# Kernel optimization log

Hardware: AMD Instinct MI355X
Metric: run time of the kernel (lower is better)

## Reference

```python
import jax, jax.numpy as jnp
import numpy as np
import math

H, C = 16, 4


def _clustering(x, alv, mu, log_var, log_prior, mi_estimation):
    # x: [B,h,L,D], alv: [B,h,L], mu/log_var: [h or 1, C, D], log_prior: [h or 1, C]
    B, Hh, L, D = x.shape
    z = x  # eval mode: no reparameterization noise
    zd = z[:, :, :, None, :]                       # [B,h,L,1,D]
    mu_b = mu[:, None, :, :]                       # [h,1,C,D]
    lv = log_var[:, None, :, :]
    var = jnp.exp(lv)
    lp = jax.nn.log_softmax(log_prior, axis=-1)    # [h,C]
    mse = (zd - mu_b) ** 2 / var                   # [B,h,L,C,D]
    log_pdf = -0.5 * mse.sum(-1) - 0.5 * lv.sum(-1) - D * math.pi  # [B,h,L,C]
    log_pdf = log_pdf + lp[:, None, :]
    shift = jax.lax.stop_gradient(log_pdf.max(axis=-1, keepdims=True))
    log_probs = jax.nn.log_softmax(log_pdf - shift + 5.0, axis=-1)
    cp = jnp.exp(log_probs)                        # cluster probs [B,h,L,C]
    lp_b = jnp.broadcast_to(lp[None, :, None, :], log_probs.shape)
    # F.kl_div(log_probs, prior) = prior * (log prior - log_probs)
    kl = (jnp.exp(lp_b) * (lp_b - log_probs)).sum(-1).mean(axis=(1, 2))
    alv5 = alv[:, :, :, None, None]
    avar = jnp.exp(alv5)
    kl = kl + 0.5 * (cp * (mse + avar / var + lv).sum(-1)).sum(-1).mean(axis=(1, 2))
    kl = kl - 0.5 * ((1.0 + alv5).sum(-1) * D).mean(axis=(1, 2, 3))
    eye = jnp.eye(L, dtype=x.dtype)
    div = jnp.einsum('bhqc,bhkc->bhqk', cp, cp)
    div = ((div - eye) ** 2) * (eye * 1.25 + (1.0 - eye) * 0.75)
    div_loss = div.mean(axis=(1, 2, 3))
    if mi_estimation:
        pdf = jnp.exp(log_pdf - jax.lax.stop_gradient(log_pdf.max())).sum(-1, keepdims=True)
        w = cp * pdf
        mi_probs = w / jnp.maximum(w.sum(axis=2, keepdims=True), 1e-6)  # L1 normalize over L
        mi_p = jnp.minimum(jnp.einsum('bilc,bjlc->blij', mi_probs, cp), 1.0)
        mask_h = 1.0 - jnp.eye(Hh, dtype=x.dtype)
        mi_loss = -(jnp.log(1.0 - mi_p + 1e-6) * mask_h).mean(axis=(1, 2, 3)) * 10.0
        aff = jnp.einsum('bhqc,bhkc->bhqk', cp, cp)
        diag = jnp.diagonal(jax.nn.log_softmax(aff, axis=-1), axis1=2, axis2=3)
        mi_loss = mi_loss - diag.mean(axis=(1, 2))
    else:
        mi_loss = jnp.zeros_like(kl)
    return z, cp, kl, div_loss, mi_loss


def _forward(query, key, value, Wq, bq, Wk, bk, Wv, bv, Wo, bo, Wsem, bsem,
             Whead, bhead, tok_mu, tok_log_var, tok_log_prior,
             head_mu, head_log_var, head_log_prior):
    B, L, D = query.shape
    Dk = D // H
    q = query @ Wq + bq
    k = key @ Wk + bk
    v = value @ Wv + bv
    alv = (q @ Wsem + bsem).transpose(0, 2, 1)                 # [B,H,L]
    qh = q.reshape(B, L, H, Dk).transpose(0, 2, 1, 3)          # [B,H,L,Dk]
    z, cp_q, kl_q, div_q, _ = _clustering(qh, alv, tok_mu, tok_log_var, tok_log_prior, False)
    kh = k.reshape(B, L, H, Dk).transpose(0, 2, 1, 3)
    vh = v.reshape(B, L, H, Dk).transpose(0, 2, 1, 3)
    cluster_mask = jnp.einsum('bhqc,bhkc->bhqk', cp_q, cp_q)   # token-cluster affinity mask
    scores = jnp.einsum('bhqd,bhkd->bhqk', z, kh) / math.sqrt(Dk)
    attn = jax.nn.softmax(scores, axis=-1) * cluster_mask
    attn = attn / (attn.sum(axis=-1, keepdims=True) + 1e-6)
    ctx = jnp.einsum('bhqk,bhkd->bhqd', attn, vh)              # [B,H,L,Dk]
    ctx_f = ctx.transpose(0, 2, 1, 3).reshape(B, L, D)
    alv_h = (ctx_f @ Whead + bhead).transpose(0, 2, 1)         # [B,H,L]
    _, cp_h, kl_h, div_h, mi = _clustering(ctx, alv_h, head_mu, head_log_var, head_log_prior, True)
    out = ctx_f @ Wo + bo
    return out, attn.mean(axis=1), kl_q + kl_h, div_q + div_h, mi


def setup_inputs() -> dict:
    key = jax.random.key(0)
    ks = jax.random.split(key, 12)
    B, L, D = 8, 512, 1024
    Dk = D // H
    s = 1.0 / math.sqrt(D)
    f32 = jnp.float32
    inp = {
        'query': jax.random.normal(ks[0], (B, L, D), f32),
        'key': jax.random.normal(ks[1], (B, L, D), f32),
        'value': jax.random.normal(ks[2], (B, L, D), f32),
        'Wq': jax.random.normal(ks[3], (D, D), f32) * s, 'bq': jnp.zeros((D,), f32),
        'Wk': jax.random.normal(ks[4], (D, D), f32) * s, 'bk': jnp.zeros((D,), f32),
        'Wv': jax.random.normal(ks[5], (D, D), f32) * s, 'bv': jnp.zeros((D,), f32),
        'Wo': jax.random.normal(ks[6], (D, D), f32) * s, 'bo': jnp.zeros((D,), f32),
        'Wsem': jax.random.normal(ks[7], (D, H), f32) * s, 'bsem': jnp.zeros((H,), f32),
        'Whead': jax.random.normal(ks[8], (D, H), f32) * s, 'bhead': jnp.zeros((H,), f32),
        'tok_mu': jax.random.normal(ks[9], (H, C, Dk), f32) * 0.1,
        'tok_log_var': jnp.zeros((H, C, Dk), f32),
        'tok_log_prior': jnp.full((H, C), math.log(1.0 / C), f32),
        'head_mu': jax.random.normal(ks[10], (1, C, Dk), f32) * 0.1,
        'head_log_var': jnp.zeros((1, C, Dk), f32),
        'head_log_prior': jnp.full((1, C), math.log(1.0 / C), f32),
    }
    return inp


def reference(query, key, value, Wq, bq, Wk, bk, Wv, bv, Wo, bo, Wsem, bsem,
              Whead, bhead, tok_mu, tok_log_var, tok_log_prior,
              head_mu, head_log_var, head_log_prior):
    return _forward(query, key, value, Wq, bq, Wk, bk, Wv, bv, Wo, bo, Wsem, bsem,
                    Whead, bhead, tok_mu, tok_log_var, tok_log_prior,
                    head_mu, head_log_var, head_log_prior)
```

## Files before the change

kernel.cpp:

```cpp
#include <hip/hip_runtime.h>
#include <math.h>

#define BB 8
#define LL 512
#define DD 1024
#define HH 16
#define CC 4
#define DK 64
#define NEG_DPI 201.06192982974676f

typedef __attribute__((ext_vector_type(8))) short short8;
typedef __attribute__((ext_vector_type(4))) float floatx4;
typedef __attribute__((ext_vector_type(8))) unsigned short u16x8;
typedef __attribute__((ext_vector_type(4))) unsigned short u16x4;

__device__ inline float block_sum256(float v, float* s_red) {
    int t = threadIdx.x;
    s_red[t] = v; __syncthreads();
    for (int off = 128; off > 0; off >>= 1) {
        if (t < off) s_red[t] += s_red[t + off];
        __syncthreads();
    }
    float r = s_red[0]; __syncthreads();
    return r;
}
__device__ inline float block_max256(float v, float* s_red) {
    int t = threadIdx.x;
    s_red[t] = v; __syncthreads();
    for (int off = 128; off > 0; off >>= 1) {
        if (t < off) s_red[t] = fmaxf(s_red[t], s_red[t + off]);
        __syncthreads();
    }
    float r = s_red[0]; __syncthreads();
    return r;
}
__device__ inline unsigned int fenc(float f) {
    unsigned int b = __float_as_uint(f);
    return (b & 0x80000000u) ? ~b : (b | 0x80000000u);
}
__device__ inline float fdec(unsigned int u) {
    return (u & 0x80000000u) ? __uint_as_float(u ^ 0x80000000u) : __uint_as_float(~u);
}
__device__ inline unsigned short f2bf(float x) {
    unsigned int u = __float_as_uint(x);
    return (unsigned short)((u + 0x7FFFu + ((u >> 16) & 1u)) >> 16);
}
__device__ inline float bf2f(unsigned short h) {
    return __uint_as_float((unsigned int)h << 16);
}

__global__ __launch_bounds__(256)
void convert_hilo(const float* __restrict__ x, unsigned short* __restrict__ hh,
                  unsigned short* __restrict__ ll) {
    int i = blockIdx.x * 256 + threadIdx.x;
    float4 v = ((const float4*)x)[i];
    u16x4 h, l;
    float c[4] = {v.x, v.y, v.z, v.w};
#pragma unroll
    for (int j = 0; j < 4; j++) {
        unsigned short hb = f2bf(c[j]);
        h[j] = hb;
        l[j] = f2bf(c[j] - bf2f(hb));
    }
    ((u16x4*)hh)[i] = h;
    ((u16x4*)ll)[i] = l;
}

__global__ __launch_bounds__(256)
void wconv_kernel(const float* __restrict__ W, unsigned short* __restrict__ Th,
                  unsigned short* __restrict__ Tl) {
    __shared__ float tile[64][65];
    int t = threadIdx.x;
    int n0 = blockIdx.x * 64, k0 = blockIdx.y * 64;
    int r = t >> 4, c4 = (t & 15) * 4;
#pragma unroll
    for (int rr = 0; rr < 64; rr += 16) {
        float4 v = *(const float4*)&W[(size_t)(k0 + r + rr) * DD + n0 + c4];
        tile[r + rr][c4 + 0] = v.x; tile[r + rr][c4 + 1] = v.y;
        tile[r + rr][c4 + 2] = v.z; tile[r + rr][c4 + 3] = v.w;
    }
    __syncthreads();
    int rn = t >> 2, kg = (t & 3) * 16;
    u16x8 oh[2], ol[2];
#pragma unroll
    for (int j = 0; j < 16; j++) {
        float x = tile[kg + j][rn];
        unsigned short hb = f2bf(x);
        oh[j >> 3][j & 7] = hb;
        ol[j >> 3][j & 7] = f2bf(x - bf2f(hb));
    }
    size_t o = (size_t)(n0 + rn) * DD + k0 + kg;
    *(u16x8*)&Th[o] = oh[0]; *(u16x8*)&Th[o + 8] = oh[1];
    *(u16x8*)&Tl[o] = ol[0]; *(u16x8*)&Tl[o + 8] = ol[1];
}

__global__ __launch_bounds__(256)
void mfma_gemm_bias(const unsigned short* __restrict__ Ah, const unsigned short* __restrict__ Al,
                    const unsigned short* __restrict__ Bh, const unsigned short* __restrict__ Bl,
                    const float* __restrict__ bias, float* __restrict__ C,
                    unsigned short* __restrict__ Ch, unsigned short* __restrict__ Cl) {
    __shared__ unsigned short sAh[128 * 32];
    __shared__ unsigned short sAl[128 * 32];
    __shared__ unsigned short sBh[128 * 32];
    __shared__ unsigned short sBl[128 * 32];
    int t = threadIdx.x;
    int n0 = blockIdx.x * 128, m0 = blockIdx.y * 128;
    int lane = t & 63, w = t >> 6;
    int wm = w >> 1, wn = w & 1;
    int lm = lane & 15, quad = lane >> 4;
    int srow = t >> 1, sk = (t & 1) * 16;

    const unsigned short* gAh = Ah + (size_t)(m0 + srow) * DD + sk;
    const unsigned short* gAl = Al + (size_t)(m0 + srow) * DD + sk;
    const unsigned short* gBh = Bh + (size_t)(n0 + srow) * DD + sk;
    const unsigned short* gBl = Bl + (size_t)(n0 + srow) * DD + sk;
    unsigned short* wAh = &sAh[srow * 32 + sk];
    unsigned short* wAl = &sAl[srow * 32 + sk];
    unsigned short* wBh = &sBh[srow * 32 + sk];
    unsigned short* wBl = &sBl[srow * 32 + sk];

    floatx4 acc[4][4] = {};

    for (int kt = 0; kt < 32; kt++) {
        int kb = kt * 32;
        u16x8 a0 = *(const u16x8*)(gAh + kb);
        u16x8 a1 = *(const u16x8*)(gAh + kb + 8);
        u16x8 a2 = *(const u16x8*)(gAl + kb);
        u16x8 a3 = *(const u16x8*)(gAl + kb + 8);
        u16x8 b0 = *(const u16x8*)(gBh + kb);
        u16x8 b1 = *(const u16x8*)(gBh + kb + 8);
        u16x8 b2 = *(const u16x8*)(gBl + kb);
        u16x8 b3 = *(const u16x8*)(gBl + kb + 8);
        __syncthreads();
        *(u16x8*)(wAh) = a0; *(u16x8*)(wAh + 8) = a1;
        *(u16x8*)(wAl) = a2; *(u16x8*)(wAl + 8) = a3;
        *(u16x8*)(wBh) = b0; *(u16x8*)(wBh + 8) = b1;
        *(u16x8*)(wBl) = b2; *(u16x8*)(wBl + 8) = b3;
        __syncthreads();

        short8 bh[4], bl[4];
#pragma unroll
        for (int j = 0; j < 4; j++) {
            int nb = (wn * 64 + j * 16 + lm) * 32 + quad * 8;
            bh[j] = *(const short8*)&sBh[nb];
            bl[j] = *(const short8*)&sBl[nb];
        }
#pragma unroll
        for (int i = 0; i < 4; i++) {
            int ab = (wm * 64 + i * 16 + lm) * 32 + quad * 8;
            short8 ah = *(const short8*)&sAh[ab];
            short8 al = *(const short8*)&sAl[ab];
#pragma unroll
            for (int j = 0; j < 4; j++) {
                acc[i][j] = __builtin_amdgcn_mfma_f32_16x16x32_bf16(ah, bh[j], acc[i][j], 0, 0, 0);
                acc[i][j] = __builtin_amdgcn_mfma_f32_16x16x32_bf16(ah, bl[j], acc[i][j], 0, 0, 0);
                acc[i][j] = __builtin_amdgcn_mfma_f32_16x16x32_bf16(al, bh[j], acc[i][j], 0, 0, 0);
            }
        }
    }
#pragma unroll
    for (int i = 0; i < 4; i++) {
#pragma unroll
        for (int j = 0; j < 4; j++) {
            int n = n0 + wn * 64 + j * 16 + lm;
            float bv = bias[n];
#pragma unroll
            for (int r = 0; r < 4; r++) {
                int m = m0 + wm * 64 + i * 16 + quad * 4 + r;
                size_t idx = (size_t)m * DD + n;
                float val = acc[i][j][r] + bv;
                if (C) C[idx] = val;
                if (Ch) {
                    unsigned short hb = f2bf(val);
                    Ch[idx] = hb;
                    Cl[idx] = f2bf(val - bf2f(hb));
                }
            }
        }
    }
}

__global__ __launch_bounds__(256)
void vt_prep(const unsigned short* __restrict__ src, unsigned short* __restrict__ dst) {
    __shared__ unsigned short tile[128 * 68];
    int t = threadIdx.x;
    int l0 = blockIdx.x * 128, h = blockIdx.y, b = blockIdx.z;
#pragma unroll
    for (int i = 0; i < 8; i++) {
        int u = t + i * 256;
        int l = u >> 4, c4 = (u & 15) * 4;
        u16x4 v4 = *(const u16x4*)&src[((size_t)(b * LL + l0 + l)) * DD + h * DK + c4];
        tile[l * 68 + c4 + 0] = v4[0]; tile[l * 68 + c4 + 1] = v4[1];
        tile[l * 68 + c4 + 2] = v4[2]; tile[l * 68 + c4 + 3] = v4[3];
    }
    __syncthreads();
    size_t ob = ((size_t)(b * HH + h)) * DK * LL;
#pragma unroll
    for (int i = 0; i < 8; i++) {
        int u = t + i * 256;
        int d = u >> 5, lq = (u & 31) * 4;
        u16x4 o;
#pragma unroll
        for (int j = 0; j < 4; j++) o[j] = tile[(lq + j) * 68 + d];
        *(u16x4*)&dst[ob + (size_t)d * LL + l0 + lq] = o;
    }
}

__global__ __launch_bounds__(256)
void alv_gemm(const float* __restrict__ A, const float* __restrict__ Wp,
              const float* __restrict__ bias, float* __restrict__ alv) {
    __shared__ float As[16][65];
    __shared__ float Ws[64][17];
    int t = threadIdx.x;
    int m0 = blockIdx.x * 16;
    int r = t >> 4, hh = t & 15;
    float acc = 0.f;
    for (int kt = 0; kt < 16; kt++) {
        __syncthreads();
#pragma unroll
        for (int i = 0; i < 4; i++) {
            int e = t + i * 256;
            int rr = e >> 6, kk = e & 63;
            As[rr][kk] = A[(size_t)(m0 + rr) * DD + kt * 64 + kk];
        }
#pragma unroll
        for (int i = 0; i < 4; i++) {
            int e = t + i * 256;
            int kk = e >> 4, h2 = e & 15;
            Ws[kk][h2] = Wp[(size_t)(kt * 64 + kk) * HH + h2];
        }
        __syncthreads();
#pragma unroll
        for (int kk = 0; kk < 64; kk++) acc += As[r][kk] * Ws[kk][hh];
    }
    int m = m0 + r;
    int b = m >> 9, l = m & 511;
    alv[(size_t)(b * HH + hh) * LL + l] = acc + bias[hh];
}

__global__ __launch_bounds__(256)
void cluster_kernel(const float* __restrict__ zsrc, const float* __restrict__ alv,
                    const float* __restrict__ mu, const float* __restrict__ logvar,
                    const float* __restrict__ logprior,
                    float* __restrict__ cp_out, float* __restrict__ lpdf_out,
                    unsigned int* __restrict__ maxenc, float* __restrict__ kl_out,
                    int isHead) {
    __shared__ float s_mu[CC * DK], s_iv[CC * DK], s_lv[CC * DK];
    __shared__ float s_slv[CC], s_siv[CC], s_lp[CC];
    __shared__ float s_red[256];
    int t = threadIdx.x;
    int tile = blockIdx.x & 1;
    int bh = blockIdx.x >> 1;
    int h = bh & (HH - 1), b = bh >> 4;
    int hm = isHead ? 0 : h;

    {
        float m = mu[hm * CC * DK + t];
        float lv = logvar[hm * CC * DK + t];
        s_mu[t] = m; s_lv[t] = lv; s_iv[t] = expf(-lv);
    }
    __syncthreads();
    if (t < CC) {
        float slv = 0.f, siv = 0.f;
        for (int d = 0; d < DK; d++) { slv += s_lv[t * DK + d]; siv += s_iv[t * DK + d]; }
        s_slv[t] = slv; s_siv[t] = siv;
    }
    if (t == CC) {
        float x[CC];
        float m = -1e30f;
        for (int c = 0; c < CC; c++) { x[c] = logprior[hm * CC + c]; m = fmaxf(m, x[c]); }
        float se = 0.f;
        for (int c = 0; c < CC; c++) se += expf(x[c] - m);
        float lse = m + logf(se);
        for (int c = 0; c < CC; c++) s_lp[c] = x[c] - lse;
    }
    __syncthreads();

    int l = tile * 256 + t;
    const float* zp = zsrc + ((size_t)(b * LL + l)) * DD + h * DK;
    float acc[CC] = {0.f, 0.f, 0.f, 0.f};
    for (int d = 0; d < DK; d += 4) {
        float4 z4 = *(const float4*)(zp + d);
#pragma unroll
        for (int c = 0; c < CC; c++) {
            float d0 = z4.x - s_mu[c * DK + d];     acc[c] += d0 * d0 * s_iv[c * DK + d];
            float d1 = z4.y - s_mu[c * DK + d + 1]; acc[c] += d1 * d1 * s_iv[c * DK + d + 1];
            float d2 = z4.z - s_mu[c * DK + d + 2]; acc[c] += d2 * d2 * s_iv[c * DK + d + 2];
            float d3 = z4.w - s_mu[c * DK + d + 3]; acc[c] += d3 * d3 * s_iv[c * DK + d + 3];
        }
    }
    float lpdf[CC];
#pragma unroll
    for (int c = 0; c < CC; c++)
        lpdf[c] = -0.5f * acc[c] - 0.5f * s_slv[c] - NEG_DPI + s_lp[c];
    float m = fmaxf(fmaxf(lpdf[0], lpdf[1]), fmaxf(lpdf[2], lpdf[3]));
    float se = 0.f;
#pragma unroll
    for (int c = 0; c < CC; c++) se += expf(lpdf[c] - m);
    float lse = m + logf(se);
    float lprob[CC], cpv[CC];
    size_t idx = ((size_t)(bh * LL + l)) * CC;
#pragma unroll
    for (int c = 0; c < CC; c++) {
        lprob[c] = lpdf[c] - lse;
        cpv[c] = expf(lprob[c]);
        cp_out[idx + c] = cpv[c];
    }
    if (isHead) {
#pragma unroll
        for (int c = 0; c < CC; c++) lpdf_out[idx + c] = lpdf[c];
    }
    float alvv = alv[(size_t)bh * LL + l];
    float avar = expf(alvv);
    float t1 = 0.f, t2 = 0.f;
#pragma unroll
    for (int c = 0; c < CC; c++) {
        t1 += expf(s_lp[c]) * (s_lp[c] - lprob[c]);
        t2 += cpv[c] * (acc[c] + avar * s_siv[c] + s_slv[c]);
    }
    float klv = t1 + 0.5f * t2 - 0.5f * (float)DK * (1.0f + alvv);
    float tot = block_sum256(klv, s_red);
    if (t == 0) atomicAdd(kl_out + b, tot * (1.0f / (HH * LL)));
    if (isHead) {
        float mt = block_max256(m, s_red);
        if (t == 0) atomicMax(maxenc, fenc(mt));
    }
}

__global__ __launch_bounds__(256)
void pairstats_kernel(const float* __restrict__ cp, float* __restrict__ div_out,
                      float* __restrict__ mi_out, int isHead) {
    __shared__ float s_cp[LL * CC];
    __shared__ float s_red[256];
    int t = threadIdx.x;
    int bh = blockIdx.x >> 3;
    int seg = blockIdx.x & 7;
    int b = bh >> 4;
    const float* base = cp + (size_t)bh * LL * CC;
#pragma unroll
    for (int i = 0; i < 2; i++) {
        int e = t + i * 256;
        *(float4*)&s_cp[e * 4] = *(const float4*)&base[e * 4];
    }
    __syncthreads();

    int q = seg * 64 + (t >> 2);
    int ln = t & 3;
    float4 cq = *(float4*)&s_cp[q * 4];
    float divacc = 0.f, m = -1e30f, s = 0.f, selfdot = 0.f;
    for (int k = ln; k < LL; k += 4) {
        float4 ck = *(float4*)&s_cp[k * 4];
        float dot = cq.x * ck.x + cq.y * ck.y + cq.z * ck.z + cq.w * ck.w;
        float del = (k == q) ? 1.f : 0.f;
        float dd = dot - del;
        divacc += dd * dd * (0.75f + 0.5f * del);
        if (isHead) {
            if (dot > m) { s = s * expf(m - dot) + 1.f; m = dot; }
            else         { s += expf(dot - m); }
            if (k == q) selfdot = dot;
        }
    }
#pragma unroll
    for (int off = 1; off <= 2; off <<= 1) divacc += __shfl_xor(divacc, off, 64);
    float diag = 0.f;
    if (isHead) {
#pragma unroll
        for (int off = 1; off <= 2; off <<= 1) {
            float om = __shfl_xor(m, off, 64);
            float os = __shfl_xor(s, off, 64);
            float nm = fmaxf(m, om);
            s = s * expf(m - nm) + os * expf(om - nm);
            m = nm;
        }
#pragma unroll
        for (int off = 1; off <= 2; off <<= 1) selfdot += __shfl_xor(selfdot, off, 64);
        diag = selfdot - (m + logf(s));
    }
    float dtot = block_sum256(ln == 0 ? divacc : 0.f, s_red);
    if (t == 0) atomicAdd(div_out + b, dtot * (1.0f / ((float)HH * LL * LL)));
    if (isHead) {
        float gtot = block_sum256(ln == 0 ? diag : 0.f, s_red);
        if (t == 0) atomicAdd(mi_out + b, -gtot * (1.0f / (HH * LL)));
    }
}

__global__ __launch_bounds__(256)
void attn3_kernel(const unsigned short* __restrict__ qoh, const unsigned short* __restrict__ qol,
                  const unsigned short* __restrict__ koh, const unsigned short* __restrict__ kol,
                  const unsigned short* __restrict__ vth, const unsigned short* __restrict__ vtl,
                  const float* __restrict__ cpq,
                  float* __restrict__ ctxf, float* __restrict__ attn_h, int h0) {
    __shared__ __align__(16) char sbuf[33280];
    __shared__ float s_cp[LL * CC];
    __shared__ float s_inv[16];
    float* S = (float*)sbuf;
    unsigned short* Ph = (unsigned short*)sbuf;
    unsigned short* Pl = Ph + 16 * 520;

    int t = threadIdx.x;
    int qt = blockIdx.x, hl = blockIdx.y, b = blockIdx.z;
    int h = h0 + hl;
    int q0 = qt * 16;
    int lane = t & 63, w = t >> 6;
    int lm = lane & 15, quad = lane >> 4;
    int bh = b * HH + h;

    {
        const float* cpb = cpq + (size_t)bh * LL * CC;
#pragma unroll
        for (int i = 0; i < 2; i++) {
            int e = t + i * 256;
            *(float4*)&s_cp[e * 4] = *(const float4*)&cpb[e * 4];
        }
    }

    size_t qbase = ((size_t)(b * LL + q0 + lm)) * DD + h * DK + quad * 8;
    short8 qah0 = *(const short8*)(qoh + qbase);
    short8 qah1 = *(const short8*)(qoh + qbase + 32);
    short8 qal0 = *(const short8*)(qol + qbase);
    short8 qal1 = *(const short8*)(qol + qbase + 32);

    floatx4 sa[8] = {};
#pragma unroll
    for (int j = 0; j < 8; j++) {
        int n0 = w * 128 + j * 16;
        size_t kbase = ((size_t)(b * LL + n0 + lm)) * DD + h * DK + quad * 8;
        short8 kbh0 = *(const short8*)(koh + kbase);
        short8 kbh1 = *(const short8*)(koh + kbase + 32);
        short8 kbl0 = *(const short8*)(kol + kbase);
        short8 kbl1 = *(const short8*)(kol + kbase + 32);
        sa[j] = __builtin_amdgcn_mfma_f32_16x16x32_bf16(qah0, kbh0, sa[j], 0, 0, 0);
        sa[j] = __builtin_amdgcn_mfma_f32_16x16x32_bf16(qah1, kbh1, sa[j], 0, 0, 0);
        sa[j] = __builtin_amdgcn_mfma_f32_16x16x32_bf16(qah0, kbl0, sa[j], 0, 0, 0);
        sa[j] = __builtin_amdgcn_mfma_f32_16x16x32_bf16(qah1, kbl1, sa[j], 0, 0, 0);
        sa[j] = __builtin_amdgcn_mfma_f32_16x16x32_bf16(qal0, kbh0, sa[j], 0, 0, 0);
        sa[j] = __builtin_amdgcn_mfma_f32_16x16x32_bf16(qal1, kbh1, sa[j], 0, 0, 0);
    }
    __syncthreads();
#pragma unroll
    for (int j = 0; j < 8; j++) {
        int kc = w * 128 + j * 16 + lm;
#pragma unroll
        for (int r = 0; r < 4; r++)
            S[(quad * 4 + r) * 516 + kc] = sa[j][r] * 0.125f;
    }
    __syncthreads();

    {
        int r = t >> 4, ln = t & 15;
        float m = -1e30f;
        for (int k = ln; k < LL; k += 16) m = fmaxf(m, S[r * 516 + k]);
#pragma unroll
        for (int off = 8; off > 0; off >>= 1) m = fmaxf(m, __shfl_xor(m, off, 16));
        float4 cq = *(float4*)&s_cp[(q0 + r) * 4];
        float Z = 0.f, Sm = 0.f;
        for (int k = ln; k < LL; k += 16) {
            float e = expf(S[r * 516 + k] - m);
            float4 ck = *(float4*)&s_cp[k * 4];
            float mask = cq.x * ck.x + cq.y * ck.y + cq.z * ck.z + cq.w * ck.w;
            float a = e * mask;
            Z += e; Sm += a;
            S[r * 516 + k] = a;
        }
#pragma unroll
        for (int off = 8; off > 0; off >>= 1) {
            Z += __shfl_xor(Z, off, 16);
            Sm += __shfl_xor(Sm, off, 16);
        }
        if (ln == 0) s_inv[r] = 1.f / (Sm + 1e-6f * Z);
    }
    __syncthreads();

    float4 pv[8];
#pragma unroll
    for (int i = 0; i < 8; i++) {
        int e = t + i * 256;
        int r2 = e >> 7, k4 = (e & 127) * 4;
        float4 p = *(float4*)&S[r2 * 516 + k4];
        float inv = s_inv[r2];
        p.x *= inv; p.y *= inv; p.z *= inv; p.w *= inv;
        pv[i] = p;
        *(float4*)&attn_h[(((size_t)((b * 8 + hl) * LL + q0 + r2)) * LL) + k4] = p;
    }
    __syncthreads();
#pragma unroll
    for (int i = 0; i < 8; i++) {
        int e = t + i * 256;
        int r2 = e >> 7, k4 = (e & 127) * 4;
        float c[4] = {pv[i].x, pv[i].y, pv[i].z, pv[i].w};
        u16x4 hv, lv;
#pragma unroll
        for (int j = 0; j < 4; j++) {
            unsigned short hb = f2bf(c[j]);
            hv[j] = hb;
            lv[j] = f2bf(c[j] - bf2f(hb));
        }
        *(u16x4*)&Ph[r2 * 520 + k4] = hv;
        *(u16x4*)&Pl[r2 * 520 + k4] = lv;
    }
    __syncthreads();

    int dn = w * 16 + lm;
    const unsigned short* vrh = vth + ((size_t)bh * DK + dn) * LL;
    const unsigned short* vrl = vtl + ((size_t)bh * DK + dn) * LL;
    floatx4 ca = {};
#pragma unroll
    for (int kc = 0; kc < 16; kc++) {
        int kb = kc * 32 + quad * 8;
        short8 pah = *(const short8*)&Ph[lm * 520 + kb];
        short8 pal = *(const short8*)&Pl[lm * 520 + kb];
        short8 vbh = *(const short8*)(vrh + kb);
        short8 vbl = *(const short8*)(vrl + kb);
        ca = __builtin_amdgcn_mfma_f32_16x16x32_bf16(pah, vbh, ca, 0, 0, 0);
        ca = __builtin_amdgcn_mfma_f32_16x16x32_bf16(pah, vbl, ca, 0, 0, 0);
        ca = __builtin_amdgcn_mfma_f32_16x16x32_bf16(pal, vbh, ca, 0, 0, 0);
    }
#pragma unroll
    for (int r = 0; r < 4; r++)
        ctxf[((size_t)(b * LL + q0 + quad * 4 + r)) * DD + h * DK + dn] = ca[r];
}

__global__ __launch_bounds__(256)
void attn_reduce(const float* __restrict__ attn_h, float* __restrict__ attn_out,
                 int accumulate) {
    int e = blockIdx.x * 256 + threadIdx.x;
    int b = e >> 16;
    int rem = e & 65535;
    float4 s = {0.f, 0.f, 0.f, 0.f};
#pragma unroll
    for (int hl = 0; hl < 8; hl++) {
        float4 v = ((const float4*)attn_h)[(((size_t)(b * 8 + hl)) << 16) + rem];
        s.x += v.x; s.y += v.y; s.z += v.z; s.w += v.w;
    }
    float4* o = (float4*)attn_out + (((size_t)b) << 16) + rem;
    const float sc = 1.0f / (float)HH;
    float4 prev = {0.f, 0.f, 0.f, 0.f};
    if (accumulate) prev = *o;
    prev.x += s.x * sc; prev.y += s.y * sc; prev.z += s.z * sc; prev.w += s.w * sc;
    *o = prev;
}

__global__ __launch_bounds__(256)
void wsum_kernel(const float* __restrict__ lpdf, const float* __restrict__ cp,
                 const unsigned int* __restrict__ maxenc,
                 float* __restrict__ pdf_out, float* __restrict__ wsum_out) {
    __shared__ float s_red[256];
    int t = threadIdx.x;
    int bh = blockIdx.x;
    float M = fdec(*maxenc);
    float a[CC] = {0.f, 0.f, 0.f, 0.f};
    for (int li = 0; li < 2; li++) {
        int l = t + li * 256;
        size_t idx = ((size_t)bh * LL + l) * CC;
        float p0 = expf(lpdf[idx + 0] - M);
        float p1 = expf(lpdf[idx + 1] - M);
        float p2 = expf(lpdf[idx + 2] - M);
        float p3 = expf(lpdf[idx + 3] - M);
        float pd = p0 + p1 + p2 + p3;
        pdf_out[(size_t)bh * LL + l] = pd;
        a[0] += cp[idx + 0] * pd; a[1] += cp[idx + 1] * pd;
        a[2] += cp[idx + 2] * pd; a[3] += cp[idx + 3] * pd;
    }
#pragma unroll
    for (int c = 0; c < CC; c++) {
        float tot = block_sum256(a[c], s_red);
        if (t == 0) wsum_out[bh * CC + c] = tot;
    }
}

__global__ __launch_bounds__(256)
void mi_kernel(const float* __restrict__ cp, const float* __restrict__ pdf,
               const float* __restrict__ wsum, float* __restrict__ mi_out) {
    __shared__ float s_q[HH * CC];
    __shared__ float s_c[HH * CC];
    __shared__ float s_red[256];
    int t = threadIdx.x;
    int b = blockIdx.x >> 9;
    int l = blockIdx.x & 511;
    if (t < HH * CC) {
        int i = t >> 2, c = t & 3;
        float cpv = cp[((size_t)(b * HH + i) * LL + l) * CC + c];
        s_c[t] = cpv;
        float w = cpv * pdf[(size_t)(b * HH + i) * LL + l];
        float ws = wsum[(b * HH + i) * CC + c];
        s_q[t] = w / fmaxf(ws, 1e-6f);
    }
    __syncthreads();
    int i = t >> 4, j = t & 15;
    float sdot = 0.f;
#pragma unroll
    for (int c = 0; c < CC; c++) sdot += s_q[i * 4 + c] * s_c[j * 4 + c];
    float mi_p = fminf(sdot, 1.f);
    float val = (i != j) ? logf(1.f - mi_p + 1e-6f) : 0.f;
    float tot = block_sum256(val, s_red);
    if (t == 0) atomicAdd(mi_out + b, -10.f * tot * (1.0f / ((float)LL * HH * HH)));
}

extern "C" void kernel_launch(void* const* d_in, const int* in_sizes, int n_in,
                              void* d_out, int out_size, void* d_ws, size_t ws_size,
                              hipStream_t stream) {
    (void)in_sizes; (void)n_in; (void)out_size; (void)ws_size;
    const float* query  = (const float*)d_in[0];
    const float* key    = (const float*)d_in[1];
    const float* value  = (const float*)d_in[2];
    const float* Wq     = (const float*)d_in[3];
    const float* bq     = (const float*)d_in[4];
    const float* Wk     = (const float*)d_in[5];
    const float* bk     = (const float*)d_in[6];
    const float* Wv     = (const float*)d_in[7];
    const float* bv     = (const float*)d_in[8];
    const float* Wo     = (const float*)d_in[9];
    const float* bo     = (const float*)d_in[10];
    const float* Wsem   = (const float*)d_in[11];
    const float* bsem   = (const float*)d_in[12];
    const float* Whead  = (const float*)d_in[13];
    const float* bhead  = (const float*)d_in[14];
    const float* tokmu  = (const float*)d_in[15];
    const float* toklv  = (const float*)d_in[16];
    const float* toklp  = (const float*)d_in[17];
    const float* headmu = (const float*)d_in[18];
    const float* headlv = (const float*)d_in[19];
    const float* headlp = (const float*)d_in[20];

    float* ws   = (float*)d_ws;
    const size_t NBLD = (size_t)BB * LL * DD;
    float* q    = ws;
    float* ctxf = ws + NBLD;
    float* alvq = ws + 2 * NBLD;
    float* alvh = alvq + (size_t)BB * HH * LL;
    float* cpq  = alvh + (size_t)BB * HH * LL;
    float* cph  = cpq + (size_t)BB * HH * LL * CC;
    float* lpdfh= cph + (size_t)BB * HH * LL * CC;
    float* pdfb = lpdfh + (size_t)BB * HH * LL * CC;
    float* wsumb= pdfb + (size_t)BB * HH * LL;
    unsigned int* maxenc = (unsigned int*)(wsumb + (size_t)BB * HH * CC);
    float* attn_h = (float*)(maxenc + 4);

    unsigned short* us = (unsigned short*)(attn_h + (size_t)BB * 8 * LL * LL);
    const size_t WSZ = (size_t)DD * DD;
    unsigned short* ist_h = us;
    unsigned short* ist_l = ist_h + NBLD;
    unsigned short* qoh = ist_l + NBLD;
    unsigned short* qol = qoh + NBLD;
    unsigned short* koh = qol + NBLD;
    unsigned short* kol = koh + NBLD;
    unsigned short* voh = kol + NBLD;
    unsigned short* vol = voh + NBLD;
    unsigned short* vth = vol + NBLD;
    unsigned short* vtl = vth + NBLD;
    unsigned short* wqh = vtl + NBLD;
    unsigned short* wql = wqh + WSZ;
    unsigned short* wkh = wql + WSZ;
    unsigned short* wkl = wkh + WSZ;
    unsigned short* wvh = wkl + WSZ;
    unsigned short* wvl = wvh + WSZ;
    unsigned short* woh = wvl + WSZ;
    unsigned short* wol = woh + WSZ;

    float* out      = (float*)d_out;
    float* attn_out = out + NBLD;
    float* kl_out   = attn_out + (size_t)BB * LL * LL;
    float* div_out  = kl_out + BB;
    float* mi_out   = div_out + BB;

    hipMemsetAsync(kl_out, 0, 3 * BB * sizeof(float), stream);
    hipMemsetAsync(maxenc, 0, sizeof(unsigned int), stream);

    dim3 wg(16, 16);
    wconv_kernel<<<wg, 256, 0, stream>>>(Wq, wqh, wql);
    wconv_kernel<<<wg, 256, 0, stream>>>(Wk, wkh, wkl);
    wconv_kernel<<<wg, 256, 0, stream>>>(Wv, wvh, wvl);
    wconv_kernel<<<wg, 256, 0, stream>>>(Wo, woh, wol);

    dim3 gg(DD / 128, BB * LL / 128);
    convert_hilo<<<NBLD / 1024, 256, 0, stream>>>(query, ist_h, ist_l);
    mfma_gemm_bias<<<gg, 256, 0, stream>>>(ist_h, ist_l, wqh, wql, bq, q, qoh, qol);
    convert_hilo<<<NBLD / 1024, 256, 0, stream>>>(key, ist_h, ist_l);
    mfma_gemm_bias<<<gg, 256, 0, stream>>>(ist_h, ist_l, wkh, wkl, bk, nullptr, koh, kol);
    convert_hilo<<<NBLD / 1024, 256, 0, stream>>>(value, ist_h, ist_l);
    mfma_gemm_bias<<<gg, 256, 0, stream>>>(ist_h, ist_l, wvh, wvl, bv, nullptr, voh, vol);

    dim3 vtg(LL / 128, HH, BB);
    vt_prep<<<vtg, 256, 0, stream>>>(voh, vth);
    vt_prep<<<vtg, 256, 0, stream>>>(vol, vtl);

    alv_gemm<<<BB * LL / 16, 256, 0, stream>>>(q, Wsem, bsem, alvq);
    cluster_kernel<<<BB * HH * 2, 256, 0, stream>>>(q, alvq, tokmu, toklv, toklp,
                                                    cpq, nullptr, nullptr, kl_out, 0);
    pairstats_kernel<<<BB * HH * 8, 256, 0, stream>>>(cpq, div_out, nullptr, 0);

    for (int h0 = 0; h0 < HH; h0 += 8) {
        attn3_kernel<<<dim3(LL / 16, 8, BB), 256, 0, stream>>>(
            qoh, qol, koh, kol, vth, vtl, cpq, ctxf, attn_h, h0);
        attn_reduce<<<BB * LL * LL / 4 / 256, 256, 0, stream>>>(
            attn_h, attn_out, h0 > 0 ? 1 : 0);
    }

    convert_hilo<<<NBLD / 1024, 256, 0, stream>>>(ctxf, ist_h, ist_l);
    alv_gemm<<<BB * LL / 16, 256, 0, stream>>>(ctxf, Whead, bhead, alvh);
    cluster_kernel<<<BB * HH * 2, 256, 0, stream>>>(ctxf, alvh, headmu, headlv, headlp,
                                                    cph, lpdfh, maxenc, kl_out, 1);
    pairstats_kernel<<<BB * HH * 8, 256, 0, stream>>>(cph, div_out, mi_out, 1);
    wsum_kernel<<<BB * HH, 256, 0, stream>>>(lpdfh, cph, maxenc, pdfb, wsumb);
    mi_kernel<<<BB * LL, 256, 0, stream>>>(cph, pdfb, wsumb, mi_out);
    mfma_gemm_bias<<<gg, 256, 0, stream>>>(ist_h, ist_l, woh, wol, bo, out, nullptr, nullptr);
}
```

Before: 837.8 us.

## Batch QKV GEMMs and weight conversions, fuse head-mean of attention into attn kernel

Merges the four weight conversions into one launch and the three QKV projection GEMMs into a single grid using blockIdx.z. The two V transpose launches become one. The attention kernel now loops over 4 heads per block and keeps the head-sum of probabilities in registers, then atomically adds the scaled result into a zeroed attn_out. This removes the large per-head attention scratch buffer writes and the separate reduce kernels, at the cost of float atomics, a memset of the output, and fewer blocks with serial head work.

Measured after the change: 915.9 us. +9.3%, slower.

```diff
diff --git a/kernel.cpp b/kernel.cpp
--- a/kernel.cpp
+++ b/kernel.cpp
@@ -67,9 +67,15 @@
 }
 
 __global__ __launch_bounds__(256)
-void wconv_kernel(const float* __restrict__ W, unsigned short* __restrict__ Th,
-                  unsigned short* __restrict__ Tl) {
+void wconv4(const float* __restrict__ W0, const float* __restrict__ W1,
+            const float* __restrict__ W2, const float* __restrict__ W3,
+            unsigned short* __restrict__ Tbase) {
     __shared__ float tile[64][65];
+    int z = blockIdx.z;
+    const float* W = (z == 0) ? W0 : (z == 1) ? W1 : (z == 2) ? W2 : W3;
+    const size_t WS = (size_t)DD * DD;
+    unsigned short* Th = Tbase + (size_t)z * 2 * WS;
+    unsigned short* Tl = Th + WS;
     int t = threadIdx.x;
     int n0 = blockIdx.x * 64, k0 = blockIdx.y * 64;
     int r = t >> 4, c4 = (t & 15) * 4;
@@ -94,11 +100,11 @@
     *(u16x8*)&Tl[o] = ol[0]; *(u16x8*)&Tl[o + 8] = ol[1];
 }
 
-__global__ __launch_bounds__(256)
-void mfma_gemm_bias(const unsigned short* __restrict__ Ah, const unsigned short* __restrict__ Al,
-                    const unsigned short* __restrict__ Bh, const unsigned short* __restrict__ Bl,
-                    const float* __restrict__ bias, float* __restrict__ C,
-                    unsigned short* __restrict__ Ch, unsigned short* __restrict__ Cl) {
+__device__ __forceinline__
+void gemm_body(const unsigned short* __restrict__ Ah, const unsigned short* __restrict__ Al,
+               const unsigned short* __restrict__ Bh, const unsigned short* __restrict__ Bl,
+               const float* __restrict__ bias, float* __restrict__ C,
+               unsigned short* __restrict__ Ch, unsigned short* __restrict__ Cl) {
     __shared__ unsigned short sAh[128 * 32];
     __shared__ unsigned short sAl[128 * 32];
     __shared__ unsigned short sBh[128 * 32];
@@ -181,10 +187,38 @@
 }
 
 __global__ __launch_bounds__(256)
-void vt_prep(const unsigned short* __restrict__ src, unsigned short* __restrict__ dst) {
+void mfma_gemm_bias(const unsigned short* __restrict__ Ah, const unsigned short* __restrict__ Al,
+                    const unsigned short* __restrict__ Bh, const unsigned short* __restrict__ Bl,
+                    const float* __restrict__ bias, float* __restrict__ C,
+                    unsigned short* __restrict__ Ch, unsigned short* __restrict__ Cl) {
+    gemm_body(Ah, Al, Bh, Bl, bias, C, Ch, Cl);
+}
+
+__global__ __launch_bounds__(256)
+void mfma_gemm_qkv(const unsigned short* __restrict__ ist3, const unsigned short* __restrict__ wbase,
+                   const float* __restrict__ bq, const float* __restrict__ bk,
+                   const float* __restrict__ bv, float* __restrict__ Cq,
+                   unsigned short* __restrict__ obase) {
+    int z = blockIdx.z;
+    const size_t NB = (size_t)BB * LL * DD;
+    const size_t WS = (size_t)DD * DD;
+    const unsigned short* Ah = ist3 + (size_t)z * 2 * NB;
+    const unsigned short* Bh = wbase + (size_t)z * 2 * WS;
+    const float* bias = (z == 0) ? bq : (z == 1) ? bk : bv;
+    float* C = (z == 0) ? Cq : nullptr;
+    unsigned short* Ch = obase + (size_t)z * 2 * NB;
+    gemm_body(Ah, Ah + NB, Bh, Bh + WS, bias, C, Ch, Ch + NB);
+}
+
+__global__ __launch_bounds__(256)
+void vt_prep2(const unsigned short* __restrict__ voh, const unsigned short* __restrict__ vol,
+              unsigned short* __restrict__ vth, unsigned short* __restrict__ vtl) {
     __shared__ unsigned short tile[128 * 68];
     int t = threadIdx.x;
-    int l0 = blockIdx.x * 128, h = blockIdx.y, b = blockIdx.z;
+    int which = blockIdx.x & 1;
+    int l0 = (blockIdx.x >> 1) * 128, h = blockIdx.y, b = blockIdx.z;
+    const unsigned short* src = which ? vol : voh;
+    unsigned short* dst = which ? vtl : vth;
 #pragma unroll
     for (int i = 0; i < 8; i++) {
         int u = t + i * 256;
@@ -384,160 +418,149 @@
     }
 }
 
-__global__ __launch_bounds__(256)
-void attn3_kernel(const unsigned short* __restrict__ qoh, const unsigned short* __restrict__ qol,
+__global__ __launch_bounds__(256, 4)
+void attn4_kernel(const unsigned short* __restrict__ qoh, const unsigned short* __restrict__ qol,
                   const unsigned short* __restrict__ koh, const unsigned short* __restrict__ kol,
                   const unsigned short* __restrict__ vth, const unsigned short* __restrict__ vtl,
                   const float* __restrict__ cpq,
-                  float* __restrict__ ctxf, float* __restrict__ attn_h, int h0) {
-    __shared__ __align__(16) char sbuf[33280];
-    __shared__ float s_cp[LL * CC];
+                  float* __restrict__ ctxf, float* __restrict__ attn_out) {
+    __shared__ __align__(16) char sbuf[33792];
     __shared__ float s_inv[16];
     float* S = (float*)sbuf;
     unsigned short* Ph = (unsigned short*)sbuf;
     unsigned short* Pl = Ph + 16 * 520;
 
     int t = threadIdx.x;
-    int qt = blockIdx.x, hl = blockIdx.y, b = blockIdx.z;
-    int h = h0 + hl;
+    int qt = blockIdx.x, hg = blockIdx.y, b = blockIdx.z;
     int q0 = qt * 16;
     int lane = t & 63, w = t >> 6;
     int lm = lane & 15, quad = lane >> 4;
-    int bh = b * HH + h;
-
-    {
-        const float* cpb = cpq + (size_t)bh * LL * CC;
-#pragma unroll
-        for (int i = 0; i < 2; i++) {
+
+    float4 pm[8] = {};
+
+#pragma unroll 1
+    for (int hi = 0; hi < 4; hi++) {
+        int h = hg * 4 + hi;
+        int bh = b * HH + h;
+
+        size_t qbase = ((size_t)(b * LL + q0 + lm)) * DD + h * DK + quad * 8;
+        short8 qah0 = *(const short8*)(qoh + qbase);
+        short8 qah1 = *(const short8*)(qoh + qbase + 32);
+        short8 qal0 = *(const short8*)(qol + qbase);
+        short8 qal1 = *(const short8*)(qol + qbase + 32);
+
+        floatx4 sa[8] = {};
+#pragma unroll
+        for (int j = 0; j < 8; j++) {
+            int n0 = w * 128 + j * 16;
+            size_t kbase = ((size_t)(b * LL + n0 + lm)) * DD + h * DK + quad * 8;
+            short8 kbh0 = *(const short8*)(koh + kbase);
+            short8 kbh1 = *(const short8*)(koh + kbase + 32);
+            short8 kbl0 = *(const short8*)(kol + kbase);
+            short8 kbl1 = *(const short8*)(kol + kbase + 32);
+            sa[j] = __builtin_amdgcn_mfma_f32_16x16x32_bf16(qah0, kbh0, sa[j], 0, 0, 0);
+            sa[j] = __builtin_amdgcn_mfma_f32_16x16x32_bf16(qah1, kbh1, sa[j], 0, 0, 0);
+            sa[j] = __builtin_amdgcn_mfma_f32_16x16x32_bf16(qah0, kbl0, sa[j], 0, 0, 0);
+            sa[j] = __builtin_amdgcn_mfma_f32_16x16x32_bf16(qah1, kbl1, sa[j], 0, 0, 0);
+            sa[j] = __builtin_amdgcn_mfma_f32_16x16x32_bf16(qal0, kbh0, sa[j], 0, 0, 0);
+            sa[j] = __builtin_amdgcn_mfma_f32_16x16x32_bf16(qal1, kbh1, sa[j], 0, 0, 0);
+        }
+        __syncthreads();
+#pragma unroll
+        for (int j = 0; j < 8; j++) {
+            int kc = w * 128 + j * 16 + lm;
+#pragma unroll
+            for (int r = 0; r < 4; r++)
+                S[(quad * 4 + r) * 528 + kc] = sa[j][r] * 0.125f;
+        }
+        __syncthreads();
+
+        {
+            int r = t >> 4, ln = t & 15;
+            const float4* cpb = (const float4*)(cpq + (size_t)bh * LL * CC);
+            float m = -1e30f;
+            for (int k = ln; k < LL; k += 16) m = fmaxf(m, S[r * 528 + k]);
+#pragma unroll
+            for (int off = 8; off > 0; off >>= 1) m = fmaxf(m, __shfl_xor(m, off, 16));
+            float4 cq = cpb[q0 + r];
+            float Z = 0.f, Sm = 0.f;
+            for (int k = ln; k < LL; k += 16) {
+                float e = expf(S[r * 528 + k] - m);
+                float4 ck = cpb[k];
+                float mask = cq.x * ck.x + cq.y * ck.y + cq.z * ck.z + cq.w * ck.w;
+                float a = e * mask;
+                Z += e; Sm += a;
+                S[r * 528 + k] = a;
+            }
+#pragma unroll
+            for (int off = 8; off > 0; off >>= 1) {
+                Z += __shfl_xor(Z, off, 16);
+                Sm += __shfl_xor(Sm, off, 16);
+            }
+            if (ln == 0) s_inv[r] = 1.f / (Sm + 1e-6f * Z);
+        }
+        __syncthreads();
+
+        float4 pv[8];
+#pragma unroll
+        for (int i = 0; i < 8; i++) {
             int e = t + i * 256;
-            *(float4*)&s_cp[e * 4] = *(const float4*)&cpb[e * 4];
-        }
-    }
-
-    size_t qbase = ((size_t)(b * LL + q0 + lm)) * DD + h * DK + quad * 8;
-    short8 qah0 = *(const short8*)(qoh + qbase);
-    short8 qah1 = *(const short8*)(qoh + qbase + 32);
-    short8 qal0 = *(const short8*)(qol + qbase);
-    short8 qal1 = *(const short8*)(qol + qbase + 32);
-
-    floatx4 sa[8] = {};
-#pragma unroll
-    for (int j = 0; j < 8; j++) {
-        int n0 = w * 128 + j * 16;
-        size_t kbase = ((size_t)(b * LL + n0 + lm)) * DD + h * DK + quad * 8;
-        short8 kbh0 = *(const short8*)(koh + kbase);
-        short8 kbh1 = *(const short8*)(koh + kbase + 32);
-        short8 kbl0 = *(const short8*)(kol + kbase);
-        short8 kbl1 = *(const short8*)(kol + kbase + 32);
-        sa[j] = __builtin_amdgcn_mfma_f32_16x16x32_bf16(qah0, kbh0, sa[j], 0, 0, 0);
-        sa[j] = __builtin_amdgcn_mfma_f32_16x16x32_bf16(qah1, kbh1, sa[j], 0, 0, 0);
-        sa[j] = __builtin_amdgcn_mfma_f32_16x16x32_bf16(qah0, kbl0, sa[j], 0, 0, 0);
-        sa[j] = __builtin_amdgcn_mfma_f32_16x16x32_bf16(qah1, kbl1, sa[j], 0, 0, 0);
-        sa[j] = __builtin_amdgcn_mfma_f32_16x16x32_bf16(qal0, kbh0, sa[j], 0, 0, 0);
-        sa[j] = __builtin_amdgcn_mfma_f32_16x16x32_bf16(qal1, kbh1, sa[j], 0, 0, 0);
-    }
-    __syncthreads();
-#pragma unroll
-    for (int j = 0; j < 8; j++) {
-        int kc = w * 128 + j * 16 + lm;
+            int r2 = e >> 7, k4 = (e & 127) * 4;
+            float4 p = *(float4*)&S[r2 * 528 + k4];
+            float inv = s_inv[r2];
+            p.x *= inv; p.y *= inv; p.z *= inv; p.w *= inv;
+            pm[i].x += p.x; pm[i].y += p.y; pm[i].z += p.z; pm[i].w += p.w;
+            pv[i] = p;
+        }
+        __syncthreads();
+#pragma unroll
+        for (int i = 0; i < 8; i++) {
+            int e = t + i * 256;
+            int r2 = e >> 7, k4 = (e & 127) * 4;
+            float c[4] = {pv[i].x, pv[i].y, pv[i].z, pv[i].w};
+            u16x4 hv, lv;
+#pragma unroll
+            for (int j = 0; j < 4; j++) {
+                unsigned short hb = f2bf(c[j]);
+                hv[j] = hb;
+                lv[j] = f2bf(c[j] - bf2f(hb));
+            }
+            *(u16x4*)&Ph[r2 * 520 + k4] = hv;
+            *(u16x4*)&Pl[r2 * 520 + k4] = lv;
+        }
+        __syncthreads();
+
+        int dn = w * 16 + lm;
+        const unsigned short* vrh = vth + ((size_t)bh * DK + dn) * LL;
+        const unsigned short* vrl = vtl + ((size_t)bh * DK + dn) * LL;
+        floatx4 ca = {};
+#pragma unroll
+        for (int kc = 0; kc < 16; kc++) {
+            int kb = kc * 32 + quad * 8;
+            short8 pah = *(const short8*)&Ph[lm * 520 + kb];
+            short8 pal = *(const short8*)&Pl[lm * 520 + kb];
+            short8 vbh = *(const short8*)(vrh + kb);
+            short8 vbl = *(const short8*)(vrl + kb);
+            ca = __builtin_amdgcn_mfma_f32_16x16x32_bf16(pah, vbh, ca, 0, 0, 0);
+            ca = __builtin_amdgcn_mfma_f32_16x16x32_bf16(pah, vbl, ca, 0, 0, 0);
+            ca = __builtin_amdgcn_mfma_f32_16x16x32_bf16(pal, vbh, ca, 0, 0, 0);
+        }
 #pragma unroll
         for (int r = 0; r < 4; r++)
-            S[(quad * 4 + r) * 516 + kc] = sa[j][r] * 0.125f;
-    }
-    __syncthreads();
-
-    {
-        int r = t >> 4, ln = t & 15;
-        float m = -1e30f;
-        for (int k = ln; k < LL; k += 16) m = fmaxf(m, S[r * 516 + k]);
-#pragma unroll
-        for (int off = 8; off > 0; off >>= 1) m = fmaxf(m, __shfl_xor(m, off, 16));
-        float4 cq = *(float4*)&s_cp[(q0 + r) * 4];
-        float Z = 0.f, Sm = 0.f;
-        for (int k = ln; k < LL; k += 16) {
-            float e = expf(S[r * 516 + k] - m);
-            float4 ck = *(float4*)&s_cp[k * 4];
-            float mask = cq.x * ck.x + cq.y * ck.y + cq.z * ck.z + cq.w * ck.w;
-            float a = e * mask;
-            Z += e; Sm += a;
-            S[r * 516 + k] = a;
-        }
-#pragma unroll
-        for (int off = 8; off > 0; off >>= 1) {
-            Z += __shfl_xor(Z, off, 16);
-            Sm += __shfl_xor(Sm, off, 16);
-        }
-        if (ln == 0) s_inv[r] = 1.f / (Sm + 1e-6f * Z);
-    }
-    __syncthreads();
-
-    float4 pv[8];
+            ctxf[((size_t)(b * LL + q0 + quad * 4 + r)) * DD + h * DK + dn] = ca[r];
+    }
+
+    const float sc = 1.0f / (float)HH;
 #pragma unroll
     for (int i = 0; i < 8; i++) {
         int e = t + i * 256;
         int r2 = e >> 7, k4 = (e & 127) * 4;
-        float4 p = *(float4*)&S[r2 * 516 + k4];
-        float inv = s_inv[r2];
-        p.x *= inv; p.y *= inv; p.z *= inv; p.w *= inv;
-        pv[i] = p;
-        *(float4*)&attn_h[(((size_t)((b * 8 + hl) * LL + q0 + r2)) * LL) + k4] = p;
-    }
-    __syncthreads();
-#pragma unroll
-    for (int i = 0; i < 8; i++) {
-        int e = t + i * 256;
-        int r2 = e >> 7, k4 = (e & 127) * 4;
-        float c[4] = {pv[i].x, pv[i].y, pv[i].z, pv[i].w};
-        u16x4 hv, lv;
-#pragma unroll
-        for (int j = 0; j < 4; j++) {
-            unsigned short hb = f2bf(c[j]);
-            hv[j] = hb;
-            lv[j] = f2bf(c[j] - bf2f(hb));
-        }
-        *(u16x4*)&Ph[r2 * 520 + k4] = hv;
-        *(u16x4*)&Pl[r2 * 520 + k4] = lv;
-    }
-    __syncthreads();
-
-    int dn = w * 16 + lm;
-    const unsigned short* vrh = vth + ((size_t)bh * DK + dn) * LL;
-    const unsigned short* vrl = vtl + ((size_t)bh * DK + dn) * LL;
-    floatx4 ca = {};
-#pragma unroll
-    for (int kc = 0; kc < 16; kc++) {
-        int kb = kc * 32 + quad * 8;
-        short8 pah = *(const short8*)&Ph[lm * 520 + kb];
-        short8 pal = *(const short8*)&Pl[lm * 520 + kb];
-        short8 vbh = *(const short8*)(vrh + kb);
-        short8 vbl = *(const short8*)(vrl + kb);
-        ca = __builtin_amdgcn_mfma_f32_16x16x32_bf16(pah, vbh, ca, 0, 0, 0);
-        ca = __builtin_amdgcn_mfma_f32_16x16x32_bf16(pah, vbl, ca, 0, 0, 0);
-        ca = __builtin_amdgcn_mfma_f32_16x16x32_bf16(pal, vbh, ca, 0, 0, 0);
-    }
-#pragma unroll
-    for (int r = 0; r < 4; r++)
-        ctxf[((size_t)(b * LL + q0 + quad * 4 + r)) * DD + h * DK + dn] = ca[r];
-}
-
-__global__ __launch_bounds__(256)
-void attn_reduce(const float* __restrict__ attn_h, float* __restrict__ attn_out,
-                 int accumulate) {
-    int e = blockIdx.x * 256 + threadIdx.x;
-    int b = e >> 16;
-    int rem = e & 65535;
-    float4 s = {0.f, 0.f, 0.f, 0.f};
-#pragma unroll
-    for (int hl = 0; hl < 8; hl++) {
-        float4 v = ((const float4*)attn_h)[(((size_t)(b * 8 + hl)) << 16) + rem];
-        s.x += v.x; s.y += v.y; s.z += v.z; s.w += v.w;
-    }
-    float4* o = (float4*)attn_out + (((size_t)b) << 16) + rem;
-    const float sc = 1.0f / (float)HH;
-    float4 prev = {0.f, 0.f, 0.f, 0.f};
-    if (accumulate) prev = *o;
-    prev.x += s.x * sc; prev.y += s.y * sc; prev.z += s.z * sc; prev.w += s.w * sc;
-    *o = prev;
+        float* dst = attn_out + ((size_t)(b * LL + q0 + r2)) * LL + k4;
+        unsafeAtomicAdd(dst + 0, pm[i].x * sc);
+        unsafeAtomicAdd(dst + 1, pm[i].y * sc);
+        unsafeAtomicAdd(dst + 2, pm[i].z * sc);
+        unsafeAtomicAdd(dst + 3, pm[i].w * sc);
+    }
 }
 
 __global__ __launch_bounds__(256)
@@ -634,9 +657,9 @@
     float* pdfb = lpdfh + (size_t)BB * HH * LL * CC;
     float* wsumb= pdfb + (size_t)BB * HH * LL;
     unsigned int* maxenc = (unsigned int*)(wsumb + (size_t)BB * HH * CC);
-    float* attn_h = (float*)(maxenc + 4);
-
-    unsigned short* us = (unsigned short*)(attn_h + (size_t)BB * 8 * LL * LL);
+    float* scr3 = (float*)(maxenc + 4);
+
+    unsigned short* us = (unsigned short*)(scr3 + (size_t)BB * 8 * LL * LL);
     const size_t WSZ = (size_t)DD * DD;
     unsigned short* ist_h = us;
     unsigned short* ist_l = ist_h + NBLD;
@@ -657,6 +680,8 @@
     unsigned short* woh = wvl + WSZ;
     unsigned short* wol = woh + WSZ;
 
+    unsigned short* ist3 = (unsigned short*)scr3;
+
     float* out      = (float*)d_out;
     float* attn_out = out + NBLD;
     float* kl_out   = attn_out + (size_t)BB * LL * LL;
@@ -665,36 +690,25 @@
 
     hipMemsetAsync(kl_out, 0, 3 * BB * sizeof(float), stream);
     hipMemsetAsync(maxenc, 0, sizeof(unsigned int), stream);
-
-    dim3 wg(16, 16);
-    wconv_kernel<<<wg, 256, 0, stream>>>(Wq, wqh, wql);
-    wconv_kernel<<<wg, 256, 0, stream>>>(Wk, wkh, wkl);
-    wconv_kernel<<<wg, 256, 0, stream>>>(Wv, wvh, wvl);
-    wconv_kernel<<<wg, 256, 0, stream>>>(Wo, woh, wol);
-
-    dim3 gg(DD / 128, BB * LL / 128);
-    convert_hilo<<<NBLD / 1024, 256, 0, stream>>>(query, ist_h, ist_l);
-    mfma_gemm_bias<<<gg, 256, 0, stream>>>(ist_h, ist_l, wqh, wql, bq, q, qoh, qol);
-    convert_hilo<<<NBLD / 1024, 256, 0, stream>>>(key, ist_h, ist_l);
-    mfma_gemm_bias<<<gg, 256, 0, stream>>>(ist_h, ist_l, wkh, wkl, bk, nullptr, koh, kol);
-    convert_hilo<<<NBLD / 1024, 256, 0, stream>>>(value, ist_h, ist_l);
-    mfma_gemm_bias<<<gg, 256, 0, stream>>>(ist_h, ist_l, wvh, wvl, bv, nullptr, voh, vol);
-
-    dim3 vtg(LL / 128, HH, BB);
-    vt_prep<<<vtg, 256, 0, stream>>>(voh, vth);
-    vt_prep<<<vtg, 256, 0, stream>>>(vol, vtl);
+    hipMemsetAsync(attn_out, 0, (size_t)BB * LL * LL * sizeof(float), stream);
+
+    wconv4<<<dim3(16, 16, 4), 256, 0, stream>>>(Wq, Wk, Wv, Wo, wqh);
+
+    convert_hilo<<<NBLD / 1024, 256, 0, stream>>>(query, ist3,            ist3 + NBLD);
+    convert_hilo<<<NBLD / 1024, 256, 0, stream>>>(key,   ist3 + 2 * NBLD, ist3 + 3 * NBLD);
+    convert_hilo<<<NBLD / 1024, 256, 0, stream>>>(value, ist3 + 4 * NBLD, ist3 + 5 * NBLD);
+    mfma_gemm_qkv<<<dim3(DD / 128, BB * LL / 128, 3), 256, 0, stream>>>(
+        ist3, wqh, bq, bk, bv, q, qoh);
+
+    vt_prep2<<<dim3(2 * LL / 128, HH, BB), 256, 0, stream>>>(voh, vol, vth, vtl);
 
     alv_gemm<<<BB * LL / 16, 256, 0, stream>>>(q, Wsem, bsem, alvq);
     cluster_kernel<<<BB * HH * 2, 256, 0, stream>>>(q, alvq, tokmu, toklv, toklp,
                                                     cpq, nullptr, nullptr, kl_out, 0);
     pairstats_kernel<<<BB * HH * 8, 256, 0, stream>>>(cpq, div_out, nullptr, 0);
 
-    for (int h0 = 0; h0 < HH; h0 += 8) {
-        attn3_kernel<<<dim3(LL / 16, 8, BB), 256, 0, stream>>>(
-            qoh, qol, koh, kol, vth, vtl, cpq, ctxf, attn_h, h0);
-        attn_reduce<<<BB * LL * LL / 4 / 256, 256, 0, stream>>>(
-            attn_h, attn_out, h0 > 0 ? 1 : 0);
-    }
+    attn4_kernel<<<dim3(LL / 16, 4, BB), 256, 0, stream>>>(
+        qoh, qol, koh, kol, vth, vtl, cpq, ctxf, attn_out);
 
     convert_hilo<<<NBLD / 1024, 256, 0, stream>>>(ctxf, ist_h, ist_l);
     alv_gemm<<<BB * LL / 16, 256, 0, stream>>>(ctxf, Whead, bhead, alvh);
@@ -703,5 +717,6 @@
     pairstats_kernel<<<BB * HH * 8, 256, 0, stream>>>(cph, div_out, mi_out, 1);
     wsum_kernel<<<BB * HH, 256, 0, stream>>>(lpdfh, cph, maxenc, pdfb, wsumb);
     mi_kernel<<<BB * LL, 256, 0, stream>>>(cph, pdfb, wsumb, mi_out);
-    mfma_gemm_bias<<<gg, 256, 0, stream>>>(ist_h, ist_l, woh, wol, bo, out, nullptr, nullptr);
-}
+    mfma_gemm_bias<<<dim3(DD / 128, BB * LL / 128), 256, 0, stream>>>(
+        ist_h, ist_l, woh, wol, bo, out, nullptr, nullptr);
+}
```
